# Kernel optimization log

Measured on AMD Instinct MI355X. Metric: run time of the kernel, lower is better.

The kernel has to match this reference:

```python
import jax, jax.numpy as jnp
import numpy as np

B, F0, D = 2048, 39, 16
LAYER_SIZES = [128, 128, 128]  # split_half=True -> field_nums [39, 64, 64]


def setup_inputs() -> dict:
    key = jax.random.key(0)
    ks = jax.random.split(key, 1 + 2 * len(LAYER_SIZES))
    inputs = jax.random.normal(ks[0], (B, F0, D), dtype=jnp.float32)
    out = {"inputs": inputs}
    field_nums = [F0]
    for i, size in enumerate(LAYER_SIZES):
        fk = field_nums[-1]
        fan_in = F0 * fk  # conv1d filter fan-in (kernel width 1)
        scale = np.sqrt(2.0 / (fan_in + size)).astype(np.float32)  # glorot
        # filter stored as [F0, Fk, size]; TF flat index is h0*Fk + hk
        out[f"w{i}"] = jax.random.normal(ks[1 + 2 * i], (F0, fk, size), dtype=jnp.float32) * scale
        out[f"b{i}"] = jnp.zeros((size,), dtype=jnp.float32)
        field_nums.append(size // 2)  # split_half=True
    return out


def reference(inputs, w0, w1, w2, b0, b1, b2):
    # CIN: per-embedding-dim outer product of x0 and x_{k-1}, then 1x1 conv
    # (shared dense over field pairs). Fused here as a single einsum per layer.
    x0 = inputs  # [B, F0, D]
    xk = inputs  # [B, Fk, D]
    params = [(w0, b0), (w1, b1), (w2, b2)]
    n_layers = len(params)
    direct = []
    for idx, (W, b) in enumerate(params):
        # out[b, s, d] = sum_{h,k} x0[b,h,d] * xk[b,k,d] * W[h,k,s]
        z = jnp.einsum('bhd,bkd,hks->bsd', x0, xk, W) + b[None, :, None]
        z = jax.nn.relu(z)  # activation='relu'
        if idx != n_layers - 1:
            half = z.shape[1] // 2  # split_half: first half feeds next layer
            xk = z[:, :half, :]
            direct.append(z[:, half:, :])
        else:
            direct.append(z)
    logit = jnp.sum(jnp.concatenate(direct, axis=1), axis=-1)  # [B, 64+64+128]
    return logit
```

## Files before the change

kernel.cpp:

```cpp
#include <hip/hip_runtime.h>
#include <stdint.h>
#include <stddef.h>

#define F0N  39
#define SN   128
#define X0TS 44
#define XKTS 72
#define WBLK 8192
#define NHB  117

typedef __attribute__((ext_vector_type(8))) short short8;
typedef __attribute__((ext_vector_type(4))) float floatx4;

__device__ __forceinline__ uint16_t f2bf(float f) {
  uint32_t u = __float_as_uint(f);
  u += 0x7fffu + ((u >> 16) & 1u);
  return (uint16_t)(u >> 16);
}

__global__ __launch_bounds__(256) void cin_prepass(
    const float* __restrict__ w0, const float* __restrict__ w1,
    const float* __restrict__ w2, uint16_t* __restrict__ wt) {
  __shared__ float T[64 * 132];
  const int bc = blockIdx.x;
  const int L = bc / F0N;
  const int h = bc - L * F0N;
  const float* W = (L == 0) ? w0 : ((L == 1) ? w1 : w2);
  const int fk = (L == 0) ? 39 : 64;
  const int tid = threadIdx.x;

  for (int e = tid; e < 8192; e += 256) {
    int k = e >> 7, s = e & 127;
    T[k * 132 + s] = (k < fk) ? W[(h * fk + k) * SN + s] : 0.0f;
  }
  __syncthreads();
  uint32_t* dst = (uint32_t*)(wt + (size_t)bc * WBLK);
  for (int i = tid; i < 4096; i += 256) {
    int frag = i >> 8, w = i & 255;
    int st = frag >> 1, ch = frag & 1;
    int ln = w >> 2, jp = w & 3;
    int quad = ln >> 4, l16 = ln & 15;
    int k0 = ch * 32 + quad * 8 + jp * 2;
    int s = st * 16 + l16;
    dst[i] = (uint32_t)f2bf(T[k0 * 132 + s]) | ((uint32_t)f2bf(T[(k0 + 1) * 132 + s]) << 16);
  }
}

__global__ __launch_bounds__(512, 2) void cin_main(
    const float* __restrict__ x,
    const float* __restrict__ bias0, const float* __restrict__ bias1,
    const float* __restrict__ bias2,
    const uint16_t* __restrict__ wt,
    float* __restrict__ out) {

  __shared__ __align__(16) float    X0T[8 * 16 * X0TS];
  __shared__ __align__(16) uint16_t XKT[8 * 16 * XKTS];

  const int tid  = threadIdx.x;
  const int lane = tid & 63;
  const int st   = tid >> 6;
  const int l16  = lane & 15;
  const int quad = lane >> 4;
  const int bbase = blockIdx.x * 8;

  {
    float* p = X0T;
#pragma unroll
    for (int i = 0; i < 11; i++) p[tid + 512 * i] = 0.f;
    uint32_t* q = (uint32_t*)XKT;
#pragma unroll
    for (int i = 0; i < 9; i++) q[tid + 512 * i] = 0u;
  }
  __syncthreads();

#pragma unroll
  for (int it = 0; it < 10; ++it) {
    int e = tid + it * 512;
    if (e < 8 * F0N * 16) {
      float v = x[(size_t)bbase * (F0N * 16) + e];
      int d = e & 15, p = e >> 4;
      int b = p / F0N, h = p - b * F0N;
      X0T[(b * 16 + d) * X0TS + h] = v;
    }
  }
  __syncthreads();

  {
    int b = tid >> 6, d = (tid >> 2) & 15, kg = tid & 3;
    const float* src = &X0T[(b * 16 + d) * X0TS];
    uint32_t* drow = (uint32_t*)&XKT[(b * 16 + d) * XKTS + kg * 16];
#pragma unroll
    for (int i2 = 0; i2 < 8; i2++) {
      int k0 = kg * 16 + i2 * 2;
      uint32_t lo = (k0 < 39)     ? (uint32_t)f2bf(src[k0])     : 0u;
      uint32_t hi = (k0 + 1 < 39) ? (uint32_t)f2bf(src[k0 + 1]) : 0u;
      drow[i2] = lo | (hi << 16);
    }
  }
  __syncthreads();

  const uint16_t* wlane = wt + st * 1024 + (size_t)lane * 8;
  const float*    xr    = &X0T[l16 * X0TS];

  short8 Wc0 = *(const short8*)(wlane);
  short8 Wc1 = *(const short8*)(wlane + 512);

#pragma unroll 1
  for (int L = 0; L < 3; ++L) {
    short8 Bf0[8], Bf1[8];
#pragma unroll
    for (int b = 0; b < 8; ++b) {
      const uint16_t* r = XKT + (b * 16 + l16) * XKTS + quad * 8;
      Bf0[b] = *(const short8*)r;
      Bf1[b] = *(const short8*)(r + 32);
    }
    const float* bp = (L == 0) ? bias0 : ((L == 1) ? bias1 : bias2);
    float bvr[4];
#pragma unroll
    for (int r = 0; r < 4; ++r) bvr[r] = bp[st * 16 + quad * 4 + r];

    floatx4 z[8] = {};
    const floatx4 zero4 = {0.f, 0.f, 0.f, 0.f};

#pragma unroll 1
    for (int h = 0; h < 40; ++h) {
      short8 Wn0, Wn1;
      {
        int Ln = L, hh = h + 1;
        if (hh >= 39) { if (L < 2) { Ln = L + 1; hh = 0; } else hh = 38; }
        const uint16_t* wl = wlane + (size_t)(Ln * F0N + hh) * WBLK;
        Wn0 = *(const short8*)wl;
        Wn1 = *(const short8*)(wl + 512);
      }

      float xs[8];
#pragma unroll
      for (int b = 0; b < 8; ++b) xs[b] = xr[b * 16 * X0TS + h];

#pragma unroll
      for (int b = 0; b < 8; ++b) {
        floatx4 y = __builtin_amdgcn_mfma_f32_16x16x32_bf16(Wc0, Bf0[b], zero4, 0, 0, 0);
        y = __builtin_amdgcn_mfma_f32_16x16x32_bf16(Wc1, Bf1[b], y, 0, 0, 0);
#pragma unroll
        for (int r = 0; r < 4; ++r) z[b][r] += xs[b] * y[r];
      }
      Wc0 = Wn0;
      Wc1 = Wn1;
    }

#pragma unroll
    for (int b = 0; b < 8; ++b) {
#pragma unroll
      for (int r = 0; r < 4; ++r) {
        float t = fmaxf(z[b][r] + bvr[r], 0.f);
        if (L < 2 && st < 4)
          XKT[(b * 16 + l16) * XKTS + st * 16 + quad * 4 + r] = f2bf(t);
        float s4 = t;
        s4 += __shfl_xor(s4, 1);
        s4 += __shfl_xor(s4, 2);
        s4 += __shfl_xor(s4, 4);
        s4 += __shfl_xor(s4, 8);
        if (l16 == 0) {
          int s = st * 16 + quad * 4 + r;
          if (L == 2)       out[(size_t)(bbase + b) * 256 + 128 + s] = s4;
          else if (s >= 64) out[(size_t)(bbase + b) * 256 + L * 64 + (s - 64)] = s4;
        }
      }
    }
    if (L < 2) __syncthreads();
  }
}

extern "C" void kernel_launch(void* const* d_in, const int* in_sizes, int n_in,
                              void* d_out, int out_size, void* d_ws, size_t ws_size,
                              hipStream_t stream) {
  (void)in_sizes; (void)n_in; (void)out_size; (void)ws_size;
  const float* x  = (const float*)d_in[0];
  const float* w0 = (const float*)d_in[1];
  const float* b0 = (const float*)d_in[2];
  const float* w1 = (const float*)d_in[3];
  const float* b1 = (const float*)d_in[4];
  const float* w2 = (const float*)d_in[5];
  const float* b2 = (const float*)d_in[6];
  uint16_t* wt    = (uint16_t*)d_ws;

  cin_prepass<<<NHB, 256, 0, stream>>>(w0, w1, w2, wt);
  cin_main<<<256, 512, 0, stream>>>(x, b0, b1, b2, wt, (float*)d_out);
}
```

Baseline: 147.5 us.

## Halve batch per block, double grid, vectorize x0 loads over four h

Each block now handles 4 batch rows instead of 8, the grid grows to 512 blocks and the launch bound asks for 4 blocks per CU. The h loop is unrolled by four so x0 scalars come from one float4 LDS read per batch row. Halving per-block state cuts register and LDS pressure, which allows more waves in flight and spreads work across more CUs. In exchange, each weight fragment is now reused across only 4 batch rows, so total weight traffic from global/L2 doubles.

```diff
diff --git a/kernel.cpp b/kernel.cpp
--- a/kernel.cpp
+++ b/kernel.cpp
@@ -4,6 +4,7 @@
 
 #define F0N  39
 #define SN   128
+#define NB   4
 #define X0TS 44
 #define XKTS 72
 #define WBLK 8192
@@ -46,37 +47,37 @@
   }
 }
 
-__global__ __launch_bounds__(512, 2) void cin_main(
+__global__ __launch_bounds__(512, 4) void cin_main(
     const float* __restrict__ x,
     const float* __restrict__ bias0, const float* __restrict__ bias1,
     const float* __restrict__ bias2,
     const uint16_t* __restrict__ wt,
     float* __restrict__ out) {
 
-  __shared__ __align__(16) float    X0T[8 * 16 * X0TS];
-  __shared__ __align__(16) uint16_t XKT[8 * 16 * XKTS];
+  __shared__ __align__(16) float    X0T[NB * 16 * X0TS];
+  __shared__ __align__(16) uint16_t XKT[NB * 16 * XKTS];
 
   const int tid  = threadIdx.x;
   const int lane = tid & 63;
   const int st   = tid >> 6;
   const int l16  = lane & 15;
   const int quad = lane >> 4;
-  const int bbase = blockIdx.x * 8;
+  const int bbase = blockIdx.x * NB;
 
   {
     float* p = X0T;
 #pragma unroll
-    for (int i = 0; i < 11; i++) p[tid + 512 * i] = 0.f;
+    for (int i = 0; i < 6; i++) { int e = tid + 512 * i; if (e < 2816) p[e] = 0.f; }
     uint32_t* q = (uint32_t*)XKT;
 #pragma unroll
-    for (int i = 0; i < 9; i++) q[tid + 512 * i] = 0u;
+    for (int i = 0; i < 5; i++) { int e = tid + 512 * i; if (e < 2304) q[e] = 0u; }
   }
   __syncthreads();
 
 #pragma unroll
-  for (int it = 0; it < 10; ++it) {
+  for (int it = 0; it < 5; ++it) {
     int e = tid + it * 512;
-    if (e < 8 * F0N * 16) {
+    if (e < NB * F0N * 16) {
       float v = x[(size_t)bbase * (F0N * 16) + e];
       int d = e & 15, p = e >> 4;
       int b = p / F0N, h = p - b * F0N;
@@ -85,7 +86,7 @@
   }
   __syncthreads();
 
-  {
+  if (tid < 256) {
     int b = tid >> 6, d = (tid >> 2) & 15, kg = tid & 3;
     const float* src = &X0T[(b * 16 + d) * X0TS];
     uint32_t* drow = (uint32_t*)&XKT[(b * 16 + d) * XKTS + kg * 16];
@@ -107,9 +108,9 @@
 
 #pragma unroll 1
   for (int L = 0; L < 3; ++L) {
-    short8 Bf0[8], Bf1[8];
+    short8 Bf0[NB], Bf1[NB];
 #pragma unroll
-    for (int b = 0; b < 8; ++b) {
+    for (int b = 0; b < NB; ++b) {
       const uint16_t* r = XKT + (b * 16 + l16) * XKTS + quad * 8;
       Bf0[b] = *(const short8*)r;
       Bf1[b] = *(const short8*)(r + 32);
@@ -119,37 +120,44 @@
 #pragma unroll
     for (int r = 0; r < 4; ++r) bvr[r] = bp[st * 16 + quad * 4 + r];
 
-    floatx4 z[8] = {};
+    floatx4 z[NB] = {};
     const floatx4 zero4 = {0.f, 0.f, 0.f, 0.f};
 
 #pragma unroll 1
-    for (int h = 0; h < 40; ++h) {
-      short8 Wn0, Wn1;
-      {
-        int Ln = L, hh = h + 1;
-        if (hh >= 39) { if (L < 2) { Ln = L + 1; hh = 0; } else hh = 38; }
-        const uint16_t* wl = wlane + (size_t)(Ln * F0N + hh) * WBLK;
-        Wn0 = *(const short8*)wl;
-        Wn1 = *(const short8*)(wl + 512);
-      }
-
-      float xs[8];
+    for (int h4 = 0; h4 < 10; ++h4) {
+      float4 xv[NB];
 #pragma unroll
-      for (int b = 0; b < 8; ++b) xs[b] = xr[b * 16 * X0TS + h];
+      for (int b = 0; b < NB; ++b)
+        xv[b] = *(const float4*)&X0T[(b * 16 + l16) * X0TS + h4 * 4];
 
 #pragma unroll
-      for (int b = 0; b < 8; ++b) {
-        floatx4 y = __builtin_amdgcn_mfma_f32_16x16x32_bf16(Wc0, Bf0[b], zero4, 0, 0, 0);
-        y = __builtin_amdgcn_mfma_f32_16x16x32_bf16(Wc1, Bf1[b], y, 0, 0, 0);
+      for (int hi = 0; hi < 4; ++hi) {
+        const int h = h4 * 4 + hi;
+        short8 Wn0, Wn1;
+        {
+          int Ln = L, hh = h + 1;
+          if (hh >= 39) { if (L < 2) { Ln = L + 1; hh = 0; } else hh = 38; }
+          const uint16_t* wl = wlane + (size_t)(Ln * F0N + hh) * WBLK;
+          Wn0 = *(const short8*)wl;
+          Wn1 = *(const short8*)(wl + 512);
+        }
+
 #pragma unroll
-        for (int r = 0; r < 4; ++r) z[b][r] += xs[b] * y[r];
+        for (int b = 0; b < NB; ++b) {
+          floatx4 y = __builtin_amdgcn_mfma_f32_16x16x32_bf16(Wc0, Bf0[b], zero4, 0, 0, 0);
+          y = __builtin_amdgcn_mfma_f32_16x16x32_bf16(Wc1, Bf1[b], y, 0, 0, 0);
+          const float xs = (hi == 0) ? xv[b].x : (hi == 1) ? xv[b].y
+                         : (hi == 2) ? xv[b].z : xv[b].w;
+#pragma unroll
+          for (int r = 0; r < 4; ++r) z[b][r] += xs * y[r];
+        }
+        Wc0 = Wn0;
+        Wc1 = Wn1;
       }
-      Wc0 = Wn0;
-      Wc1 = Wn1;
     }
 
 #pragma unroll
-    for (int b = 0; b < 8; ++b) {
+    for (int b = 0; b < NB; ++b) {
 #pragma unroll
       for (int r = 0; r < 4; ++r) {
         float t = fmaxf(z[b][r] + bvr[r], 0.f);
@@ -185,5 +193,5 @@
   uint16_t* wt    = (uint16_t*)d_ws;
 
   cin_prepass<<<NHB, 256, 0, stream>>>(w0, w1, w2, wt);
-  cin_main<<<256, 512, 0, stream>>>(x, b0, b1, b2, wt, (float*)d_out);
+  cin_main<<<512, 512, 0, stream>>>(x, b0, b1, b2, wt, (float*)d_out);
 }
```

Measured after the change: 144.3 us. 2.2% less time.
